# Kernel optimization log

Hardware: AMD Instinct MI355X
Metric: run time of the kernel (lower is better)

The kernel has to match this reference:

```python
import jax, jax.numpy as jnp
import numpy as np

IGNORE_INDEX = -100
LABEL_SMOOTHING = 0.0
BT, H, V = 4096, 2048, 32000


def setup_inputs() -> dict:
    key = jax.random.key(0)
    k1, k2, k3, k4 = jax.random.split(key, 4)
    x = jax.random.normal(k1, (BT, H), dtype=jnp.float32)
    target = jax.random.randint(k2, (BT,), 0, V, dtype=jnp.int64)
    weight = jax.random.normal(k3, (V, H), dtype=jnp.float32) * 0.02
    bias = jax.random.normal(k4, (V,), dtype=jnp.float32) * 0.02
    return {"x": x, "target": target, "weight": weight, "bias": bias}


def reference(x, target, weight, bias):
    # logits: [BT, V] — the module avoids materializing this by chunking;
    # as a correctness reference we compute it directly.
    logits = jnp.einsum('th,vh->tv', x, weight) + bias
    lse = jax.nn.logsumexp(logits, axis=-1)                      # [BT]
    tgt_logit = jnp.take_along_axis(logits, target[:, None], axis=-1)[:, 0]
    valid = target != IGNORE_INDEX
    total = jnp.maximum(valid.sum(), 1).astype(logits.dtype)
    per_tok = -(tgt_logit - lse)                                 # hard-label NLL
    if LABEL_SMOOTHING > 0.0:
        eps = LABEL_SMOOTHING / V
        per_tok = per_tok * (1.0 - LABEL_SMOOTHING) + (
            -eps * logits.sum(axis=-1) + LABEL_SMOOTHING * lse)
    per_tok = jnp.where(valid, per_tok, 0.0)
    # reduction == 'mean': divide by number of non-ignored targets
    loss = per_tok.sum() / total
    return loss
```

## Files before the change

kernel.cpp:

```cpp
#include <hip/hip_runtime.h>
#include <cstdint>

#define BT 4096
#define H  2048
#define V  32000
#define BM 256
#define BN 256
#define BK 128
#define NRT (BT/BM)
#define NVT (V/BN)
#define PJ  128
#define WSCALE 64.0f
#define INV_WSCALE 0.015625f

typedef int   v8i   __attribute__((ext_vector_type(8)));
typedef float f32x4 __attribute__((ext_vector_type(4)));
typedef float f4v   __attribute__((ext_vector_type(4)));

__device__ __forceinline__ void async_load16(const void* g, void* l) {
    __builtin_amdgcn_global_load_lds(
        (__attribute__((address_space(1))) uint32_t*)(void*)g,
        (__attribute__((address_space(3))) uint32_t*)l, 16, 0, 0);
}

__global__ void quant_all(const float* __restrict__ X, const float* __restrict__ W,
                          int* __restrict__ Xq, int* __restrict__ Wq,
                          float* __restrict__ accum) {
    const int NX = BT * H / 4;
    const int NW = (int)((size_t)V * H / 4);
    int i = blockIdx.x * blockDim.x + threadIdx.x;
    if (i == 0) { accum[0] = 0.f; accum[1] = 0.f; }
    if (i < NX) {
        f4v v = __builtin_nontemporal_load((const f4v*)X + i);
        int p = __builtin_amdgcn_cvt_pk_fp8_f32(v.x, v.y, 0, false);
        p     = __builtin_amdgcn_cvt_pk_fp8_f32(v.z, v.w, p, true);
        Xq[i] = p;
    } else if (i < NX + NW) {
        int j = i - NX;
        f4v v = __builtin_nontemporal_load((const f4v*)W + j);
        int p = __builtin_amdgcn_cvt_pk_fp8_f32(v.x * WSCALE, v.y * WSCALE, 0, false);
        p     = __builtin_amdgcn_cvt_pk_fp8_f32(v.z * WSCALE, v.w * WSCALE, p, true);
        Wq[j] = p;
    }
}

__global__ __launch_bounds__(512, 2) void gemm_lse(
    const uint8_t* __restrict__ Xq,
    const uint8_t* __restrict__ Wq,
    const float* __restrict__ bias,
    const int*  __restrict__ target,
    float* __restrict__ part_m,
    float* __restrict__ part_l,
    float* __restrict__ tgt_logit)
{
    __shared__ __align__(16) uint8_t smem[131072];

    const int tid  = threadIdx.x;
    const int lane = tid & 63;
    const int wave = tid >> 6;
    const int wm   = wave >> 2;
    const int wn   = wave & 3;

    const int bid = blockIdx.x;
    const int swz = (bid & 7) * 250 + (bid >> 3);
    const int rbk = swz & 15;
    const int cbk = swz >> 4;
    const int row0 = rbk * BM;
    const int col0 = cbk * BN;

    f32x4 acc[8][4];
#pragma unroll
    for (int i = 0; i < 8; i++)
#pragma unroll
        for (int j = 0; j < 4; j++) acc[i][j] = (f32x4){0.f, 0.f, 0.f, 0.f};

    const int srow   = lane >> 3;
    const int schunk = ((lane & 7) ^ srow) * 16;
    const uint8_t* Aptr = Xq + (size_t)(row0 + 32 * wave + srow) * H + schunk;
    const uint8_t* Bptr = Wq + (size_t)(col0 + 32 * wave + srow) * H + schunk;

    auto stage = [&](int buf, const uint8_t* ap_, const uint8_t* bp_) {
        uint8_t* as_ = smem + buf * 65536;
        uint8_t* bs_ = smem + buf * 65536 + 32768;
#pragma unroll
        for (int L = 0; L < 4; L++) {
            const int g = 4 * wave + L;
            async_load16(ap_ + (size_t)(8 * L) * H, as_ + g * 1024);
            async_load16(bp_ + (size_t)(8 * L) * H, bs_ + g * 1024);
        }
    };

    stage(0, Aptr, Bptr);
    __syncthreads();

    const int lr  = lane & 15;
    const int g32 = lane >> 4;

    union Frag { int4 q[2]; v8i v; };

    for (int t = 0; t < H / BK; ++t) {
        const int cur = t & 1;
        if (t < H / BK - 1) {
            Aptr += BK; Bptr += BK;
            stage(cur ^ 1, Aptr, Bptr);
        }
        const uint8_t* As = smem + cur * 65536;
        const uint8_t* Bs = smem + cur * 65536 + 32768;

        auto lda = [&](int i, Frag& f) {
            const int r  = wm * 128 + i * 16 + lr;
            const int p0 = (2 * g32) ^ (r & 7);
            const int4* base = (const int4*)&As[r * BK];
            f.q[0] = base[p0];
            f.q[1] = base[p0 ^ 1];
        };

        Frag bf[4];
#pragma unroll
        for (int j = 0; j < 4; j++) {
            const int r  = wn * 64 + j * 16 + lr;
            const int p0 = (2 * g32) ^ (r & 7);
            const int4* base = (const int4*)&Bs[r * BK];
            bf[j].q[0] = base[p0];
            bf[j].q[1] = base[p0 ^ 1];
        }

        Frag a0, a1, n0, n1;
        lda(0, a0);
        lda(1, a1);
#pragma unroll
        for (int q = 0; q < 4; q++) {
            if (q < 3) {
                lda(2 * q + 2, n0);
                lda(2 * q + 3, n1);
            }
            __builtin_amdgcn_s_setprio(1);
#pragma unroll
            for (int j = 0; j < 4; j++)
                acc[2 * q][j] = __builtin_amdgcn_mfma_scale_f32_16x16x128_f8f6f4(
                    a0.v, bf[j].v, acc[2 * q][j],
                    0, 0, 0, 0x7f7f7f7f, 0, 0x7f7f7f7f);
#pragma unroll
            for (int j = 0; j < 4; j++)
                acc[2 * q + 1][j] = __builtin_amdgcn_mfma_scale_f32_16x16x128_f8f6f4(
                    a1.v, bf[j].v, acc[2 * q + 1][j],
                    0, 0, 0, 0x7f7f7f7f, 0, 0x7f7f7f7f);
            __builtin_amdgcn_s_setprio(0);
            a0 = n0;
            a1 = n1;
        }
        __syncthreads();
    }

    float* red_m = (float*)smem;
    float* red_l = (float*)(smem + 4096);
    int*   tgts  = (int*)(smem + 8192);

    if (tid < 256) tgts[tid] = target[row0 + tid];
    __syncthreads();

    const int quad = lane >> 4;
    float bj[4];
#pragma unroll
    for (int j = 0; j < 4; j++) bj[j] = bias[col0 + wn * 64 + j * 16 + lr];

#pragma unroll
    for (int i = 0; i < 8; i++) {
#pragma unroll
        for (int r = 0; r < 4; r++) {
            const int rit = wm * 128 + i * 16 + quad * 4 + r;
            float v[4];
#pragma unroll
            for (int j = 0; j < 4; j++) v[j] = acc[i][j][r] * INV_WSCALE + bj[j];
            const int tg = tgts[rit];
#pragma unroll
            for (int j = 0; j < 4; j++)
                if (col0 + wn * 64 + j * 16 + lr == tg)
                    tgt_logit[row0 + rit] = v[j];
            float mx = fmaxf(fmaxf(v[0], v[1]), fmaxf(v[2], v[3]));
#pragma unroll
            for (int d = 1; d < 16; d <<= 1) mx = fmaxf(mx, __shfl_xor(mx, d));
            float se = __expf(v[0] - mx) + __expf(v[1] - mx) +
                       __expf(v[2] - mx) + __expf(v[3] - mx);
#pragma unroll
            for (int d = 1; d < 16; d <<= 1) se += __shfl_xor(se, d);
            if (lr == 0) { red_m[wn * 256 + rit] = mx; red_l[wn * 256 + rit] = se; }
        }
    }
    __syncthreads();
    if (tid < 256) {
        float M = red_m[tid];
        float m1 = red_m[256 + tid], m2 = red_m[512 + tid], m3 = red_m[768 + tid];
        M = fmaxf(fmaxf(M, m1), fmaxf(m2, m3));
        float L = red_l[tid]       * __expf(red_m[tid]       - M)
                + red_l[256 + tid] * __expf(m1 - M)
                + red_l[512 + tid] * __expf(m2 - M)
                + red_l[768 + tid] * __expf(m3 - M);
        part_m[(size_t)(row0 + tid) * PJ + cbk] = M;
        part_l[(size_t)(row0 + tid) * PJ + cbk] = L;
    }
}

__global__ void finalize(const float* __restrict__ part_m,
                         const float* __restrict__ part_l,
                         const float* __restrict__ tgt_logit,
                         const int*  __restrict__ target,
                         float* __restrict__ accum)
{
    const int wave = threadIdx.x >> 6, lane = threadIdx.x & 63;
    const int t = blockIdx.x * 4 + wave;
    float m[2], l[2];
#pragma unroll
    for (int c = 0; c < 2; c++) {
        const int j = c * 64 + lane;
        const bool ok = j < NVT;
        m[c] = ok ? part_m[(size_t)t * PJ + j] : -1e30f;
        l[c] = ok ? part_l[(size_t)t * PJ + j] : 0.f;
    }
    float M = fmaxf(m[0], m[1]);
#pragma unroll
    for (int d = 1; d < 64; d <<= 1) M = fmaxf(M, __shfl_xor(M, d));
    float S = l[0] * __expf(m[0] - M) + l[1] * __expf(m[1] - M);
#pragma unroll
    for (int d = 1; d < 64; d <<= 1) S += __shfl_xor(S, d);

    __shared__ float sm[4], sc[4];
    if (lane == 0) {
        const int tg = target[t];
        float loss = 0.f, cnt = 0.f;
        if (tg != -100) {
            loss = (M + __logf(S)) - tgt_logit[t];
            cnt  = 1.f;
        }
        sm[wave] = loss; sc[wave] = cnt;
    }
    __syncthreads();
    if (threadIdx.x == 0) {
        float Ls = sm[0] + sm[1] + sm[2] + sm[3];
        float Cs = sc[0] + sc[1] + sc[2] + sc[3];
        atomicAdd(&accum[0], Ls);
        atomicAdd(&accum[1], Cs);
    }
}

__global__ void final_div(const float* __restrict__ accum, float* __restrict__ out) {
    out[0] = accum[0] / fmaxf(accum[1], 1.f);
}

extern "C" void kernel_launch(void* const* d_in, const int* in_sizes, int n_in,
                              void* d_out, int out_size, void* d_ws, size_t ws_size,
                              hipStream_t stream) {
    const float* x      = (const float*)d_in[0];
    const int*   target = (const int*)d_in[1];
    const float* w      = (const float*)d_in[2];
    const float* bias   = (const float*)d_in[3];

    char* ws = (char*)d_ws;
    size_t off = 0;
    auto alloc = [&](size_t bytes) {
        void* p = ws + off;
        off += (bytes + 255) & ~(size_t)255;
        return p;
    };
    uint8_t* Xq   = (uint8_t*)alloc((size_t)BT * H);
    uint8_t* Wq   = (uint8_t*)alloc((size_t)V * H);
    float* part_m = (float*)alloc((size_t)BT * PJ * 4);
    float* part_l = (float*)alloc((size_t)BT * PJ * 4);
    float* tgtl   = (float*)alloc((size_t)BT * 4);
    float* accum  = (float*)alloc(256);

    const int nq = BT * H / 4 + (int)((size_t)V * H / 4);
    quant_all<<<(nq + 255) / 256, 256, 0, stream>>>(
        x, w, (int*)Xq, (int*)Wq, accum);

    gemm_lse<<<NRT * NVT, 512, 0, stream>>>(Xq, Wq, bias, target, part_m, part_l, tgtl);

    finalize<<<BT / 4, 256, 0, stream>>>(part_m, part_l, tgtl, target, accum);

    final_div<<<1, 1, 0, stream>>>(accum, (float*)d_out);
}
```

Baseline: 735.7 us.

## Interleave split A/B prefetch with MFMA phases using explicit waitcnt and barriers

```diff
diff --git a/kernel.cpp b/kernel.cpp
--- a/kernel.cpp
+++ b/kernel.cpp
@@ -7,6 +7,7 @@
 #define BM 256
 #define BN 256
 #define BK 128
+#define NT (H/BK)
 #define NRT (BT/BM)
 #define NVT (V/BN)
 #define PJ  128
@@ -79,31 +80,32 @@
     const uint8_t* Aptr = Xq + (size_t)(row0 + 32 * wave + srow) * H + schunk;
     const uint8_t* Bptr = Wq + (size_t)(col0 + 32 * wave + srow) * H + schunk;
 
-    auto stage = [&](int buf, const uint8_t* ap_, const uint8_t* bp_) {
+    auto stageA = [&](int buf) {
         uint8_t* as_ = smem + buf * 65536;
+#pragma unroll
+        for (int L = 0; L < 4; L++)
+            async_load16(Aptr + (size_t)(8 * L) * H, as_ + (4 * wave + L) * 1024);
+    };
+    auto stageB = [&](int buf) {
         uint8_t* bs_ = smem + buf * 65536 + 32768;
 #pragma unroll
-        for (int L = 0; L < 4; L++) {
-            const int g = 4 * wave + L;
-            async_load16(ap_ + (size_t)(8 * L) * H, as_ + g * 1024);
-            async_load16(bp_ + (size_t)(8 * L) * H, bs_ + g * 1024);
-        }
+        for (int L = 0; L < 4; L++)
+            async_load16(Bptr + (size_t)(8 * L) * H, bs_ + (4 * wave + L) * 1024);
     };
 
-    stage(0, Aptr, Bptr);
-    __syncthreads();
+    stageA(0); stageB(0);
+    Aptr += BK; Bptr += BK;
+    asm volatile("s_waitcnt vmcnt(0)" ::: "memory");
+    __builtin_amdgcn_s_barrier();
 
     const int lr  = lane & 15;
     const int g32 = lane >> 4;
 
     union Frag { int4 q[2]; v8i v; };
 
-    for (int t = 0; t < H / BK; ++t) {
+    for (int t = 0; t < NT; ++t) {
         const int cur = t & 1;
-        if (t < H / BK - 1) {
-            Aptr += BK; Bptr += BK;
-            stage(cur ^ 1, Aptr, Bptr);
-        }
+        const bool pf = (t < NT - 1);
         const uint8_t* As = smem + cur * 65536;
         const uint8_t* Bs = smem + cur * 65536 + 32768;
 
@@ -117,39 +119,45 @@
 
         Frag bf[4];
 #pragma unroll
-        for (int j = 0; j < 4; j++) {
-            const int r  = wn * 64 + j * 16 + lr;
-            const int p0 = (2 * g32) ^ (r & 7);
-            const int4* base = (const int4*)&Bs[r * BK];
-            bf[j].q[0] = base[p0];
-            bf[j].q[1] = base[p0 ^ 1];
-        }
-
-        Frag a0, a1, n0, n1;
-        lda(0, a0);
-        lda(1, a1);
-#pragma unroll
-        for (int q = 0; q < 4; q++) {
-            if (q < 3) {
-                lda(2 * q + 2, n0);
-                lda(2 * q + 3, n1);
+        for (int p = 0; p < 4; ++p) {
+            Frag a0, a1;
+            lda(2 * p,     a0);
+            lda(2 * p + 1, a1);
+            if (p == 0) {
+#pragma unroll
+                for (int j = 0; j < 4; j++) {
+                    const int r  = wn * 64 + j * 16 + lr;
+                    const int p0 = (2 * g32) ^ (r & 7);
+                    const int4* base = (const int4*)&Bs[r * BK];
+                    bf[j].q[0] = base[p0];
+                    bf[j].q[1] = base[p0 ^ 1];
+                }
+                if (pf) stageA(cur ^ 1);
+                asm volatile("s_waitcnt lgkmcnt(8)" ::: "memory");
             }
+            if (p == 1 && pf) stageB(cur ^ 1);
+            __builtin_amdgcn_s_barrier();
+            asm volatile("s_waitcnt lgkmcnt(0)" ::: "memory");
+            __builtin_amdgcn_sched_barrier(0);
             __builtin_amdgcn_s_setprio(1);
 #pragma unroll
             for (int j = 0; j < 4; j++)
-                acc[2 * q][j] = __builtin_amdgcn_mfma_scale_f32_16x16x128_f8f6f4(
-                    a0.v, bf[j].v, acc[2 * q][j],
+                acc[2 * p][j] = __builtin_amdgcn_mfma_scale_f32_16x16x128_f8f6f4(
+                    a0.v, bf[j].v, acc[2 * p][j],
                     0, 0, 0, 0x7f7f7f7f, 0, 0x7f7f7f7f);
 #pragma unroll
             for (int j = 0; j < 4; j++)
-                acc[2 * q + 1][j] = __builtin_amdgcn_mfma_scale_f32_16x16x128_f8f6f4(
-                    a1.v, bf[j].v, acc[2 * q + 1][j],
+                acc[2 * p + 1][j] = __builtin_amdgcn_mfma_scale_f32_16x16x128_f8f6f4(
+                    a1.v, bf[j].v, acc[2 * p + 1][j],
                     0, 0, 0, 0x7f7f7f7f, 0, 0x7f7f7f7f);
             __builtin_amdgcn_s_setprio(0);
-            a0 = n0;
-            a1 = n1;
-        }
-        __syncthreads();
+            if (p < 3) __builtin_amdgcn_s_barrier();
+        }
+        if (pf) {
+            Aptr += BK; Bptr += BK;
+            asm volatile("s_waitcnt vmcnt(0)" ::: "memory");
+        }
+        __builtin_amdgcn_s_barrier();
     }
 
     float* red_m = (float*)smem;
```

New measurement: 733.8 us. No clear change (-0.3%).
